# Optimization experiments

Hardware: AMD Instinct MI355X
Metric: run time of the kernel (lower is better)

## Reference

```python
import jax, jax.numpy as jnp
import numpy as np

B, T, D_IN, H, D_OUT = 64, 512, 256, 1024, 256


def _gru_cell(x, h, Wi, Wh, bi, bh):
    # x: [B, in_dim], h: [B, H]; Wi: [3H, in_dim], Wh: [3H, H]
    gi = x @ Wi.T + bi  # [B, 3H]
    gh = h @ Wh.T + bh  # [B, 3H]
    i_r, i_z, i_n = jnp.split(gi, 3, axis=-1)
    h_r, h_z, h_n = jnp.split(gh, 3, axis=-1)
    r = jax.nn.sigmoid(i_r + h_r)
    z = jax.nn.sigmoid(i_z + h_z)
    n = jnp.tanh(i_n + r * h_n)
    return (1.0 - z) * n + z * h


def setup_inputs() -> dict:
    key = jax.random.key(0)
    ks = jax.random.split(key, 11)
    s_in = 1.0 / np.sqrt(D_IN)
    s_h = 1.0 / np.sqrt(H)
    return {
        "x": jax.random.normal(ks[0], (B, T, D_IN), jnp.float32),
        "Wi0": jax.random.normal(ks[1], (3 * H, D_IN), jnp.float32) * s_in,
        "Wh0": jax.random.normal(ks[2], (3 * H, H), jnp.float32) * s_h,
        "bi0": jax.random.normal(ks[3], (3 * H,), jnp.float32) * s_h,
        "bh0": jax.random.normal(ks[4], (3 * H,), jnp.float32) * s_h,
        "Wi1": jax.random.normal(ks[5], (3 * H, H), jnp.float32) * s_h,
        "Wh1": jax.random.normal(ks[6], (3 * H, H), jnp.float32) * s_h,
        "bi1": jax.random.normal(ks[7], (3 * H,), jnp.float32) * s_h,
        "bh1": jax.random.normal(ks[8], (3 * H,), jnp.float32) * s_h,
        "Wo": jax.random.normal(ks[9], (D_OUT, H), jnp.float32) * s_h,
        "bo": jax.random.normal(ks[10], (D_OUT,), jnp.float32) * s_h,
    }


def reference(x, Wi0, Wh0, bi0, bh0, Wi1, Wh1, bi1, bh1, Wo, bo):
    b = x.shape[0]
    h0 = jnp.zeros((b, H), x.dtype)
    h1 = jnp.zeros((b, H), x.dtype)

    def step(carry, x_t):
        h0, h1 = carry
        h0 = _gru_cell(x_t, h0, Wi0, Wh0, bi0, bh0)
        h1 = _gru_cell(h0, h1, Wi1, Wh1, bi1, bh1)
        return (h0, h1), None

    (h0, h1), _ = jax.lax.scan(step, (h0, h1), jnp.swapaxes(x, 0, 1))
    return h1 @ Wo.T + bo  # [B, D_OUT]
```

## Files before the change

### kernel.cpp

```cpp
#include <hip/hip_runtime.h>

constexpr int kB    = 64;
constexpr int kT    = 512;
constexpr int kDin  = 256;
constexpr int kH    = 1024;
constexpr int kH3   = 3072;
constexpr int kDout = 256;
constexpr int kHB   = kB * kH;

typedef float  f32x4  __attribute__((ext_vector_type(4)));
typedef __bf16 bf16x8 __attribute__((ext_vector_type(8)));
typedef unsigned u32x4 __attribute__((ext_vector_type(4)));
typedef unsigned long long u64;

__device__ __forceinline__ float b2f(unsigned short u) {
  union { float f; unsigned u32; } c; c.u32 = ((unsigned)u) << 16; return c.f;
}
__device__ __forceinline__ unsigned short f2b(float f) {
  union { float f; unsigned u32; } c; c.f = f;
  unsigned r = c.u32 + 0x7fffu + ((c.u32 >> 16) & 1u);
  return (unsigned short)(r >> 16);
}
__device__ __forceinline__ bf16x8 ld8(const unsigned short* p) {
  return *reinterpret_cast<const bf16x8*>(p);
}
__device__ __forceinline__ u64 ald(const u64* p) {
  return __hip_atomic_load(p, __ATOMIC_RELAXED, __HIP_MEMORY_SCOPE_AGENT);
}
__device__ __forceinline__ unsigned ald32(const unsigned* p) {
  return __hip_atomic_load(p, __ATOMIC_RELAXED, __HIP_MEMORY_SCOPE_AGENT);
}
__device__ __forceinline__ void ast32(unsigned* p, unsigned v) {
  __hip_atomic_store(p, v, __ATOMIC_RELAXED, __HIP_MEMORY_SCOPE_AGENT);
}
__device__ __forceinline__ float sigm_(float x) { return 1.f / (1.f + __expf(-x)); }
__device__ __forceinline__ float tanh_(float x) {
  return 1.f - 2.f / (__expf(2.f * x) + 1.f);
}

#define MFMA16(a, b, c) __builtin_amdgcn_mfma_f32_16x16x32_bf16((a), (b), (c), 0, 0, 0)

__device__ __forceinline__ int swzcol(int C, int quad) {
  return (C & ~63) + ((quad ^ (((C >> 3) ^ (C >> 6)) & 7)) << 3);
}

__global__ void gru_prep(const float* __restrict__ x,
                         const float* __restrict__ Wi0, const float* __restrict__ Wh0,
                         const float* __restrict__ bi0, const float* __restrict__ bh0,
                         const float* __restrict__ Wi1, const float* __restrict__ Wh1,
                         const float* __restrict__ bi1, const float* __restrict__ bh1,
                         unsigned short* __restrict__ xb,
                         unsigned short* __restrict__ wi0b, unsigned short* __restrict__ wh0b,
                         unsigned short* __restrict__ wi1b, unsigned short* __restrict__ wh1b,
                         unsigned short* __restrict__ r0, unsigned short* __restrict__ r1,
                         float* __restrict__ bias, unsigned* __restrict__ sync) {
  const int stride = gridDim.x * blockDim.x;
  const int g = blockIdx.x * blockDim.x + threadIdx.x;
  for (int i = g; i < kH3 * kDin; i += stride) wi0b[i] = f2b(Wi0[i]);
  for (int i = g; i < kH3 * kH; i += stride) {
    wh0b[i] = f2b(Wh0[i]); wi1b[i] = f2b(Wi1[i]); wh1b[i] = f2b(Wh1[i]);
  }
  for (int i = g; i < kB * kT * kDin; i += stride) xb[i] = f2b(x[i]);
  for (int i = g; i < kHB; i += stride) { r0[i] = 0; r1[i] = 0; }
  for (int i = g; i < kH; i += stride) {
    bias[0 * kH + i] = bi0[0 * kH + i] + bh0[0 * kH + i];
    bias[1 * kH + i] = bi0[1 * kH + i] + bh0[1 * kH + i];
    bias[2 * kH + i] = bi0[2 * kH + i];
    bias[3 * kH + i] = bh0[2 * kH + i];
    bias[4 * kH + i] = bi1[0 * kH + i] + bh1[0 * kH + i];
    bias[5 * kH + i] = bi1[1 * kH + i] + bh1[1 * kH + i];
    bias[6 * kH + i] = bi1[2 * kH + i];
    bias[7 * kH + i] = bh1[2 * kH + i];
  }
  for (int i = g; i < 4096; i += stride) sync[i] = 0;
}

__global__ void __launch_bounds__(256, 1) gru_main(
    const unsigned short* __restrict__ xb,
    const unsigned short* __restrict__ wi0, const unsigned short* __restrict__ wh0,
    const unsigned short* __restrict__ wi1, const unsigned short* __restrict__ wh1,
    const float* __restrict__ bias,
    unsigned short* __restrict__ r0, unsigned short* __restrict__ r1,
    unsigned* __restrict__ sync, const int rmode,
    const float* __restrict__ Wo, const float* __restrict__ bo,
    float* __restrict__ out) {
  __shared__ unsigned short hl0[16][1032];
  __shared__ unsigned short hl1[16][1032];
  __shared__ float red[2][4][64][5];
  __shared__ bf16x8 wlds[2][32][64];

  const int tid  = threadIdx.x;
  const int lane = tid & 63;
  const int wv   = tid >> 6;
  const int ln15 = lane & 15;
  const int quad = lane >> 4;

  const int xcd   = blockIdx.x & 7;
  const int rest  = blockIdx.x >> 3;
  const int jsub  = rest & 7;
  const int mtile = rest >> 3;
  const int pidx  = xcd * 8 + jsub;

  const int layer = wv >> 1;
  const int kh    = wv & 1;
  const int jrow  = xcd * 128 + jsub * 16 + ln15;
  const int jcol  = jrow;

  const unsigned short *pw_r, *pw_z, *pw_n, *pv_r, *pv_z, *pv_n;
  if (layer == 0) {
    pw_r = wh0 + (size_t)(0 * kH + jrow) * kH + kh * 512 + quad * 8;
    pw_z = wh0 + (size_t)(1 * kH + jrow) * kH + kh * 512 + quad * 8;
    pw_n = wh0 + (size_t)(2 * kH + jrow) * kH + kh * 512 + quad * 8;
    pv_r = wi0 + (size_t)(0 * kH + jrow) * kDin + kh * 128 + quad * 8;
    pv_z = wi0 + (size_t)(1 * kH + jrow) * kDin + kh * 128 + quad * 8;
    pv_n = wi0 + (size_t)(2 * kH + jrow) * kDin + kh * 128 + quad * 8;
  } else {
    pw_r = wh1 + (size_t)(0 * kH + jrow) * kH + kh * 512 + quad * 8;
    pw_z = wh1 + (size_t)(1 * kH + jrow) * kH + kh * 512 + quad * 8;
    pw_n = wh1 + (size_t)(2 * kH + jrow) * kH + kh * 512 + quad * 8;
    pv_r = wi1 + (size_t)(0 * kH + jrow) * kH + kh * 512 + quad * 8;
    pv_z = wi1 + (size_t)(1 * kH + jrow) * kH + kh * 512 + quad * 8;
    pv_n = wi1 + (size_t)(2 * kH + jrow) * kH + kh * 512 + quad * 8;
  }

  const float* bb = bias + layer * 4 * kH;
  const float b_r = bb[jcol];
  const float b_z = bb[kH + jcol];
  const float b_i = bb[2 * kH + jcol];
  const float b_h = bb[3 * kH + jcol];

  bf16x8 W[64];
  if (layer == 0) {
#pragma unroll
    for (int kk = 0; kk < 16; ++kk) {
      W[kk]      = ld8(pw_r + kk * 32);
      W[16 + kk] = ld8(pw_z + kk * 32);
      W[32 + kk] = ld8(pw_n + kk * 32);
    }
#pragma unroll
    for (int kk = 0; kk < 4; ++kk) {
      W[48 + kk] = ld8(pv_r + kk * 32);
      W[52 + kk] = ld8(pv_z + kk * 32);
      W[56 + kk] = ld8(pv_n + kk * 32);
    }
  } else {
#pragma unroll
    for (int kk = 0; kk < 16; ++kk) {
      W[kk]      = ld8(pv_r + kk * 32);
      W[16 + kk] = ld8(pv_z + kk * 32);
      W[32 + kk] = ld8(pv_n + kk * 32);
      W[48 + kk] = ld8(pw_r + kk * 32);
      wlds[kh][kk][lane]      = ld8(pw_z + kk * 32);
      wlds[kh][16 + kk][lane] = ld8(pw_n + kk * 32);
    }
  }

  const f32x4 z4 = {0.f, 0.f, 0.f, 0.f};
  unsigned* fl0 = sync + (size_t)xcd * 512 + mtile * 64;
  unsigned* fl1 = sync + (size_t)xcd * 512 + 256 + mtile * 64;

  float hprev[4] = {0.f, 0.f, 0.f, 0.f};

  for (int t = 0; t <= kT; ++t) {
    const bool l0c = (t < kT);
    const bool l1c = (t >= 1);
    const int s0r = rmode ? t : (t & 1);
    const int s0w = rmode ? (t + 1) : ((t + 1) & 1);
    const int s1r = rmode ? (t >= 1 ? t - 1 : 0) : ((t >= 1 ? t - 1 : 0) & 1);
    const int s1w = rmode ? t : (t & 1);

    f32x4 a_r = z4, a_z = z4, a_i = z4, a_h = z4;

    if (layer == 0 && l0c) {
      const unsigned short* xp = xb + (size_t)(mtile * 16 + ln15) * (kT * kDin) +
                                 t * kDin + kh * 128 + quad * 8;
      bf16x8 xa[4];
#pragma unroll
      for (int i = 0; i < 4; ++i) xa[i] = ld8(xp + i * 32);
#pragma unroll
      for (int kk = 0; kk < 4; ++kk) {
        a_r = MFMA16(xa[kk], W[48 + kk], a_r);
        a_z = MFMA16(xa[kk], W[52 + kk], a_z);
        a_i = MFMA16(xa[kk], W[56 + kk], a_i);
      }
    }

    if (wv == 0) {
      int missed = 0;
      for (;;) {
        int a = (int)ald32(fl0 + lane);
        int b = (int)ald32(fl1 + lane);
        if (__all(a >= t && b >= t - 1)) break;
        if (!missed) { __builtin_amdgcn_s_sleep(16); missed = 1; }
        else         { __builtin_amdgcn_s_sleep(4); }
      }
    }
    __syncthreads();

    {
      const int r = tid >> 4, s = tid & 15;
      const unsigned short* b0 =
          r0 + (size_t)s0r * kHB + (size_t)(mtile * 16 + r) * kH + s * 64;
      const unsigned short* b1 =
          r1 + (size_t)s1r * kHB + (size_t)(mtile * 16 + r) * kH + s * 64;
      if (rmode) {
        u32x4 d0[8], d1[8];
#pragma unroll
        for (int i = 0; i < 8; ++i) d0[i] = *(const u32x4*)(b0 + i * 8);
#pragma unroll
        for (int i = 0; i < 8; ++i) d1[i] = *(const u32x4*)(b1 + i * 8);
#pragma unroll
        for (int i = 0; i < 8; ++i)
          *(u32x4*)&hl0[r][s * 64 + ((i ^ s) & 7) * 8] = d0[i];
#pragma unroll
        for (int i = 0; i < 8; ++i)
          *(u32x4*)&hl1[r][s * 64 + ((i ^ s) & 7) * 8] = d1[i];
      } else {
        u64 w0[16], w1[16];
#pragma unroll
        for (int i = 0; i < 16; ++i) w0[i] = ald((const u64*)b0 + i);
#pragma unroll
        for (int i = 0; i < 16; ++i) w1[i] = ald((const u64*)b1 + i);
#pragma unroll
        for (int i = 0; i < 16; ++i)
          *(u64*)&hl0[r][s * 64 + (((i >> 1) ^ s) & 7) * 8 + (i & 1) * 4] = w0[i];
#pragma unroll
        for (int i = 0; i < 16; ++i)
          *(u64*)&hl1[r][s * 64 + (((i >> 1) ^ s) & 7) * 8 + (i & 1) * 4] = w1[i];
      }
    }
    __syncthreads();

    const bool active = (layer == 0) ? l0c : l1c;
    if (active) {
      const int kb = kh * 512;
      if (layer == 0) {
#pragma unroll
        for (int kk = 0; kk < 16; ++kk) {
          bf16x8 A = *(const bf16x8*)&hl0[ln15][swzcol(kb + kk * 32, quad)];
          a_r = MFMA16(A, W[kk], a_r);
          a_z = MFMA16(A, W[16 + kk], a_z);
          a_h = MFMA16(A, W[32 + kk], a_h);
        }
      } else {
#pragma unroll
        for (int kk = 0; kk < 16; ++kk) {
          bf16x8 A0 = *(const bf16x8*)&hl0[ln15][swzcol(kb + kk * 32, quad)];
          a_r = MFMA16(A0, W[kk], a_r);
          a_z = MFMA16(A0, W[16 + kk], a_z);
          a_i = MFMA16(A0, W[32 + kk], a_i);
          bf16x8 A1 = *(const bf16x8*)&hl1[ln15][swzcol(kb + kk * 32, quad)];
          a_r = MFMA16(A1, W[48 + kk], a_r);
          a_z = MFMA16(A1, wlds[kh][kk][lane], a_z);
          a_h = MFMA16(A1, wlds[kh][16 + kk][lane], a_h);
        }
      }
    }

    if (((wv == 1) && l0c) || ((wv == 3) && l1c)) {
#pragma unroll
      for (int q = 0; q < 4; ++q) {
        red[layer][0][lane][q] = a_r[q]; red[layer][1][lane][q] = a_z[q];
        red[layer][2][lane][q] = a_i[q]; red[layer][3][lane][q] = a_h[q];
      }
    }
    __syncthreads();

    if (((wv == 0) && l0c) || ((wv == 2) && l1c)) {
      float hv4[4];
#pragma unroll
      for (int q = 0; q < 4; ++q) {
        float sr = a_r[q] + red[layer][0][lane][q];
        float sz = a_z[q] + red[layer][1][lane][q];
        float si = a_i[q] + red[layer][2][lane][q];
        float sh = a_h[q] + red[layer][3][lane][q];
        float rg = sigm_(sr + b_r);
        float zg = sigm_(sz + b_z);
        float ng = tanh_(si + b_i + rg * (sh + b_h));
        hv4[q] = (1.f - zg) * ng + zg * hprev[q];
        hprev[q] = hv4[q];
      }
      unsigned short* dst = (layer == 0) ? r0 + (size_t)s0w * kHB
                                         : r1 + (size_t)s1w * kHB;
#pragma unroll
      for (int q = 0; q < 4; ++q) {
        float pv = __shfl_xor(hv4[q], 1);
        if (!(lane & 1)) {
          unsigned pk = (unsigned)f2b(hv4[q]) | ((unsigned)f2b(pv) << 16);
          unsigned* d = (unsigned*)(dst + (size_t)(mtile * 16 + quad * 4 + q) * kH +
                                    (jcol & ~1));
          ast32(d, pk);
        }
      }
      asm volatile("s_waitcnt vmcnt(0)" ::: "memory");
      if (lane == 0) {
        const int base = (layer == 0) ? (mtile * 64 + pidx)
                                      : (256 + mtile * 64 + pidx);
        const unsigned val = (layer == 0) ? (unsigned)(t + 1) : (unsigned)t;
#pragma unroll
        for (int r8 = 0; r8 < 8; ++r8) ast32(sync + r8 * 512 + base, val);
      }
    }
  }

  if (wv == 0) {
    int missed = 0;
    for (;;) {
      int f = (int)ald32(fl1 + lane);
      if (__all(f >= (int)kT)) break;
      if (!missed) { __builtin_amdgcn_s_sleep(16); missed = 1; }
      else         { __builtin_amdgcn_s_sleep(4); }
    }
  }
  __syncthreads();
  {
    const int sfin = rmode ? kT : 0;
    const int r = tid >> 4, s = tid & 15;
    const unsigned short* b1 =
        r1 + (size_t)sfin * kHB + (size_t)(mtile * 16 + r) * kH + s * 64;
    if (rmode) {
      u32x4 d[8];
#pragma unroll
      for (int i = 0; i < 8; ++i) d[i] = *(const u32x4*)(b1 + i * 8);
#pragma unroll
      for (int i = 0; i < 8; ++i) *(u32x4*)&hl0[r][s * 64 + i * 8] = d[i];
    } else {
      u64 w[16];
#pragma unroll
      for (int i = 0; i < 16; ++i) w[i] = ald((const u64*)b1 + i);
#pragma unroll
      for (int i = 0; i < 16; ++i) *(u64*)&hl0[r][s * 64 + i * 4] = w[i];
    }
  }
  __syncthreads();
  {
    const int c  = tid & 31;
    const int rr = tid >> 5;
    const int col = jsub * 32 + c;
    const float* wr = Wo + (size_t)col * kH;
    float acc0 = bo[col], acc1 = bo[col];
#pragma unroll 8
    for (int k = 0; k < kH; k += 4) {
      float4 w4 = *reinterpret_cast<const float4*>(wr + k);
      acc0 += b2f(hl0[rr][k]) * w4.x + b2f(hl0[rr][k + 1]) * w4.y +
              b2f(hl0[rr][k + 2]) * w4.z + b2f(hl0[rr][k + 3]) * w4.w;
      acc1 += b2f(hl0[rr + 8][k]) * w4.x + b2f(hl0[rr + 8][k + 1]) * w4.y +
              b2f(hl0[rr + 8][k + 2]) * w4.z + b2f(hl0[rr + 8][k + 3]) * w4.w;
    }
    out[(mtile * 16 + rr) * kDout + col] = acc0;
    out[(mtile * 16 + rr + 8) * kDout + col] = acc1;
  }
}

extern "C" void kernel_launch(void* const* d_in, const int* in_sizes, int n_in,
                              void* d_out, int out_size, void* d_ws, size_t ws_size,
                              hipStream_t stream) {
  const float* x   = (const float*)d_in[0];
  const float* Wi0 = (const float*)d_in[1];
  const float* Wh0 = (const float*)d_in[2];
  const float* bi0 = (const float*)d_in[3];
  const float* bh0 = (const float*)d_in[4];
  const float* Wi1 = (const float*)d_in[5];
  const float* Wh1 = (const float*)d_in[6];
  const float* bi1 = (const float*)d_in[7];
  const float* bh1 = (const float*)d_in[8];
  const float* Wo  = (const float*)d_in[9];
  const float* bo  = (const float*)d_in[10];

  char* ws = (char*)d_ws;
  size_t off = 0;
  auto take = [&](size_t bytes) {
    size_t r = off;
    off += (bytes + 255) & ~(size_t)255;
    return r;
  };
  unsigned short* xb   = (unsigned short*)(ws + take((size_t)kB * kT * kDin * 2));
  unsigned short* wi0b = (unsigned short*)(ws + take((size_t)kH3 * kDin * 2));
  unsigned short* wh0b = (unsigned short*)(ws + take((size_t)kH3 * kH * 2));
  unsigned short* wi1b = (unsigned short*)(ws + take((size_t)kH3 * kH * 2));
  unsigned short* wh1b = (unsigned short*)(ws + take((size_t)kH3 * kH * 2));
  float*          bias = (float*)(ws + take(8 * kH * sizeof(float)));
  unsigned*       sync = (unsigned*)(ws + take(4096 * sizeof(unsigned)));

  const size_t slot_b = (size_t)kHB * 2;
  int rmode = 1;
  size_t ring_slots = (size_t)kT + 1;
  if (off + 2 * (ring_slots * slot_b) + (1u << 20) > ws_size) {
    rmode = 0;
    ring_slots = 2;
  }
  unsigned short* r0 = (unsigned short*)(ws + take(ring_slots * slot_b));
  unsigned short* r1 = (unsigned short*)(ws + take(ring_slots * slot_b));

  gru_prep<<<2048, 256, 0, stream>>>(x, Wi0, Wh0, bi0, bh0, Wi1, Wh1, bi1, bh1,
                                     xb, wi0b, wh0b, wi1b, wh1b, r0, r1, bias,
                                     sync);
  gru_main<<<256, 256, 0, stream>>>(xb, wi0b, wh0b, wi1b, wh1b, bias, r0, r1,
                                    sync, rmode, Wo, bo, (float*)d_out);
}
```

Before: 3.319 ms.

## Tile hidden-state buffers per producer block and poll flags in every wave

Changes the global layout of the recurrent hidden-state ring buffers so each producer block writes a contiguous 16x16 tile (mtile*16384 + pidx*256) instead of strided rows. The staging into LDS is rewritten to read these tiles with a matching swizzle. Every wave now spins on the sync flags itself, which removes the __syncthreads that followed the wave-0 poll, and the sleep intervals are shortened. Flag publication uses eight lanes in parallel instead of a serial loop in lane 0. The aim is to cut per-step synchronisation latency and get coalesced remote stores. The cost is more polling traffic from all waves and a swizzle that must stay consistent with the MFMA reads.

```diff
diff --git a/kernel.cpp b/kernel.cpp
--- a/kernel.cpp
+++ b/kernel.cpp
@@ -42,6 +42,42 @@
 
 __device__ __forceinline__ int swzcol(int C, int quad) {
   return (C & ~63) + ((quad ^ (((C >> 3) ^ (C >> 6)) & 7)) << 3);
+}
+
+__device__ __forceinline__ void stage_p(unsigned short (*hl)[1032],
+                                        const unsigned short* slotm,
+                                        int p, int rg, int rmode) {
+  const unsigned short* src = slotm + p * 256 + rg * 64;
+  const int cb = p * 2;
+  if (rmode) {
+    u32x4 d[8];
+#pragma unroll
+    for (int i = 0; i < 4; ++i) {
+      d[i * 2]     = *(const u32x4*)(src + i * 16);
+      d[i * 2 + 1] = *(const u32x4*)(src + i * 16 + 8);
+    }
+#pragma unroll
+    for (int i = 0; i < 4; ++i)
+#pragma unroll
+      for (int h = 0; h < 2; ++h) {
+        const int c  = cb + h;
+        const int so = ((c & ~7) | ((c ^ (c >> 3)) & 7)) * 8;
+        *(u32x4*)&hl[rg * 4 + i][so] = d[i * 2 + h];
+      }
+  } else {
+    u64 w[16];
+#pragma unroll
+    for (int i = 0; i < 16; ++i) w[i] = ald((const u64*)src + i);
+#pragma unroll
+    for (int i = 0; i < 4; ++i)
+#pragma unroll
+      for (int h = 0; h < 2; ++h) {
+        const int c  = cb + h;
+        const int so = ((c & ~7) | ((c ^ (c >> 3)) & 7)) * 8;
+        *(u64*)&hl[rg * 4 + i][so]     = w[i * 4 + h * 2];
+        *(u64*)&hl[rg * 4 + i][so + 4] = w[i * 4 + h * 2 + 1];
+      }
+  }
 }
 
 __global__ void gru_prep(const float* __restrict__ x,
@@ -161,6 +197,9 @@
 
   float hprev[4] = {0.f, 0.f, 0.f, 0.f};
 
+  const int sp  = tid & 63;
+  const int srg = tid >> 6;
+
   for (int t = 0; t <= kT; ++t) {
     const bool l0c = (t < kT);
     const bool l1c = (t >= 1);
@@ -185,50 +224,19 @@
       }
     }
 
-    if (wv == 0) {
-      int missed = 0;
+    {
+      int first = 1;
       for (;;) {
         int a = (int)ald32(fl0 + lane);
         int b = (int)ald32(fl1 + lane);
         if (__all(a >= t && b >= t - 1)) break;
-        if (!missed) { __builtin_amdgcn_s_sleep(16); missed = 1; }
-        else         { __builtin_amdgcn_s_sleep(4); }
-      }
-    }
-    __syncthreads();
-
-    {
-      const int r = tid >> 4, s = tid & 15;
-      const unsigned short* b0 =
-          r0 + (size_t)s0r * kHB + (size_t)(mtile * 16 + r) * kH + s * 64;
-      const unsigned short* b1 =
-          r1 + (size_t)s1r * kHB + (size_t)(mtile * 16 + r) * kH + s * 64;
-      if (rmode) {
-        u32x4 d0[8], d1[8];
-#pragma unroll
-        for (int i = 0; i < 8; ++i) d0[i] = *(const u32x4*)(b0 + i * 8);
-#pragma unroll
-        for (int i = 0; i < 8; ++i) d1[i] = *(const u32x4*)(b1 + i * 8);
-#pragma unroll
-        for (int i = 0; i < 8; ++i)
-          *(u32x4*)&hl0[r][s * 64 + ((i ^ s) & 7) * 8] = d0[i];
-#pragma unroll
-        for (int i = 0; i < 8; ++i)
-          *(u32x4*)&hl1[r][s * 64 + ((i ^ s) & 7) * 8] = d1[i];
-      } else {
-        u64 w0[16], w1[16];
-#pragma unroll
-        for (int i = 0; i < 16; ++i) w0[i] = ald((const u64*)b0 + i);
-#pragma unroll
-        for (int i = 0; i < 16; ++i) w1[i] = ald((const u64*)b1 + i);
-#pragma unroll
-        for (int i = 0; i < 16; ++i)
-          *(u64*)&hl0[r][s * 64 + (((i >> 1) ^ s) & 7) * 8 + (i & 1) * 4] = w0[i];
-#pragma unroll
-        for (int i = 0; i < 16; ++i)
-          *(u64*)&hl1[r][s * 64 + (((i >> 1) ^ s) & 7) * 8 + (i & 1) * 4] = w1[i];
-      }
-    }
+        if (first) { __builtin_amdgcn_s_sleep(8); first = 0; }
+        else       { __builtin_amdgcn_s_sleep(2); }
+      }
+    }
+
+    stage_p(hl0, r0 + (size_t)s0r * kHB + mtile * 16384, sp, srg, rmode);
+    stage_p(hl1, r1 + (size_t)s1r * kHB + mtile * 16384, sp, srg, rmode);
     __syncthreads();
 
     const bool active = (layer == 0) ? l0c : l1c;
@@ -280,56 +288,63 @@
         hv4[q] = (1.f - zg) * ng + zg * hprev[q];
         hprev[q] = hv4[q];
       }
-      unsigned short* dst = (layer == 0) ? r0 + (size_t)s0w * kHB
-                                         : r1 + (size_t)s1w * kHB;
+      unsigned short* dst = ((layer == 0) ? r0 + (size_t)s0w * kHB
+                                          : r1 + (size_t)s1w * kHB) +
+                            mtile * 16384 + pidx * 256;
 #pragma unroll
       for (int q = 0; q < 4; ++q) {
         float pv = __shfl_xor(hv4[q], 1);
         if (!(lane & 1)) {
           unsigned pk = (unsigned)f2b(hv4[q]) | ((unsigned)f2b(pv) << 16);
-          unsigned* d = (unsigned*)(dst + (size_t)(mtile * 16 + quad * 4 + q) * kH +
-                                    (jcol & ~1));
+          unsigned* d = (unsigned*)(dst + (quad * 4 + q) * 16 + (ln15 & ~1));
           ast32(d, pk);
         }
       }
       asm volatile("s_waitcnt vmcnt(0)" ::: "memory");
-      if (lane == 0) {
-        const int base = (layer == 0) ? (mtile * 64 + pidx)
-                                      : (256 + mtile * 64 + pidx);
-        const unsigned val = (layer == 0) ? (unsigned)(t + 1) : (unsigned)t;
-#pragma unroll
-        for (int r8 = 0; r8 < 8; ++r8) ast32(sync + r8 * 512 + base, val);
-      }
-    }
-  }
-
-  if (wv == 0) {
-    int missed = 0;
+      const int base = (layer == 0) ? (mtile * 64 + pidx)
+                                    : (256 + mtile * 64 + pidx);
+      const unsigned val = (layer == 0) ? (unsigned)(t + 1) : (unsigned)t;
+      if (lane < 8) ast32(sync + lane * 512 + base, val);
+    }
+  }
+
+  {
+    int first = 1;
     for (;;) {
       int f = (int)ald32(fl1 + lane);
       if (__all(f >= (int)kT)) break;
-      if (!missed) { __builtin_amdgcn_s_sleep(16); missed = 1; }
-      else         { __builtin_amdgcn_s_sleep(4); }
+      if (first) { __builtin_amdgcn_s_sleep(8); first = 0; }
+      else       { __builtin_amdgcn_s_sleep(2); }
     }
   }
   __syncthreads();
   {
     const int sfin = rmode ? kT : 0;
-    const int r = tid >> 4, s = tid & 15;
-    const unsigned short* b1 =
-        r1 + (size_t)sfin * kHB + (size_t)(mtile * 16 + r) * kH + s * 64;
+    const unsigned short* src =
+        r1 + (size_t)sfin * kHB + mtile * 16384 + sp * 256 + srg * 64;
     if (rmode) {
       u32x4 d[8];
 #pragma unroll
-      for (int i = 0; i < 8; ++i) d[i] = *(const u32x4*)(b1 + i * 8);
-#pragma unroll
-      for (int i = 0; i < 8; ++i) *(u32x4*)&hl0[r][s * 64 + i * 8] = d[i];
+      for (int i = 0; i < 4; ++i) {
+        d[i * 2]     = *(const u32x4*)(src + i * 16);
+        d[i * 2 + 1] = *(const u32x4*)(src + i * 16 + 8);
+      }
+#pragma unroll
+      for (int i = 0; i < 4; ++i) {
+        *(u32x4*)&hl0[srg * 4 + i][sp * 16]     = d[i * 2];
+        *(u32x4*)&hl0[srg * 4 + i][sp * 16 + 8] = d[i * 2 + 1];
+      }
     } else {
       u64 w[16];
 #pragma unroll
-      for (int i = 0; i < 16; ++i) w[i] = ald((const u64*)b1 + i);
-#pragma unroll
-      for (int i = 0; i < 16; ++i) *(u64*)&hl0[r][s * 64 + i * 4] = w[i];
+      for (int i = 0; i < 16; ++i) w[i] = ald((const u64*)src + i);
+#pragma unroll
+      for (int i = 0; i < 4; ++i) {
+        *(u64*)&hl0[srg * 4 + i][sp * 16]      = w[i * 4];
+        *(u64*)&hl0[srg * 4 + i][sp * 16 + 4]  = w[i * 4 + 1];
+        *(u64*)&hl0[srg * 4 + i][sp * 16 + 8]  = w[i * 4 + 2];
+        *(u64*)&hl0[srg * 4 + i][sp * 16 + 12] = w[i * 4 + 3];
+      }
     }
   }
   __syncthreads();
```

Measured after the change: 3.438 ms. 3.6% more time.

## Replace block-wide barriers with per-wave LDS flag handoffs in GRU time loop

Applied to the files above, without the earlier changes.

Removes the three __syncthreads per timestep and replaces them with fine-grained LDS producer/consumer flags between the four waves. Each wave now polls global sync flags itself and stages only its half of the hidden state. Layer-0 and layer-1 waves can therefore run decoupled within a step. In rmode, the global flag wait checks only the relevant 32 producer slots instead of all 64, and the sleep intervals are shortened. The risks are more complex ordering, duplicated polling traffic, and subtle races on the LDS buffers shared between layers.

```diff
diff --git a/kernel.cpp b/kernel.cpp
--- a/kernel.cpp
+++ b/kernel.cpp
@@ -42,6 +42,45 @@
 
 __device__ __forceinline__ int swzcol(int C, int quad) {
   return (C & ~63) + ((quad ^ (((C >> 3) ^ (C >> 6)) & 7)) << 3);
+}
+
+__device__ __forceinline__ void stage_seg(unsigned short* ldsrow,
+                                          const unsigned short* src, int s,
+                                          int rmode) {
+  if (rmode) {
+    u32x4 d[8];
+#pragma unroll
+    for (int i = 0; i < 8; ++i) d[i] = *(const u32x4*)(src + i * 8);
+#pragma unroll
+    for (int i = 0; i < 8; ++i)
+      *(u32x4*)&ldsrow[s * 64 + ((i ^ s) & 7) * 8] = d[i];
+  } else {
+    u64 w[16];
+#pragma unroll
+    for (int i = 0; i < 16; ++i) w[i] = ald((const u64*)src + i);
+#pragma unroll
+    for (int i = 0; i < 16; ++i)
+      *(u64*)&ldsrow[s * 64 + (((i >> 1) ^ s) & 7) * 8 + (i & 1) * 4] = w[i];
+  }
+}
+
+__device__ __forceinline__ void stage_half(unsigned short (*hl)[1032],
+                                           const unsigned short* rbase,
+                                           int kh, int lane, int rmode) {
+  const int r = lane >> 2;
+  const int s = kh * 8 + (lane & 3) * 2;
+  const unsigned short* src = rbase + (size_t)r * kH + s * 64;
+  stage_seg(hl[r], src, s, rmode);
+  stage_seg(hl[r], src + 64, s + 1, rmode);
+}
+
+__device__ __forceinline__ void pb_post(unsigned* p, unsigned v, int lane) {
+  if (lane == 0)
+    __hip_atomic_store(p, v, __ATOMIC_RELEASE, __HIP_MEMORY_SCOPE_WORKGROUP);
+}
+__device__ __forceinline__ void pb_wait(unsigned* p, unsigned v) {
+  while (__hip_atomic_load(p, __ATOMIC_ACQUIRE, __HIP_MEMORY_SCOPE_WORKGROUP) < v)
+    __builtin_amdgcn_s_sleep(1);
 }
 
 __global__ void gru_prep(const float* __restrict__ x,
@@ -88,6 +127,7 @@
   __shared__ unsigned short hl1[16][1032];
   __shared__ float red[2][4][64][5];
   __shared__ bf16x8 wlds[2][32][64];
+  __shared__ unsigned pb[8];
 
   const int tid  = threadIdx.x;
   const int lane = tid & 63;
@@ -155,6 +195,9 @@
     }
   }
 
+  if (tid < 8) pb[tid] = 0;
+  __syncthreads();
+
   const f32x4 z4 = {0.f, 0.f, 0.f, 0.f};
   unsigned* fl0 = sync + (size_t)xcd * 512 + mtile * 64;
   unsigned* fl1 = sync + (size_t)xcd * 512 + 256 + mtile * 64;
@@ -169,72 +212,46 @@
     const int s1r = rmode ? (t >= 1 ? t - 1 : 0) : ((t >= 1 ? t - 1 : 0) & 1);
     const int s1w = rmode ? t : (t & 1);
 
-    f32x4 a_r = z4, a_z = z4, a_i = z4, a_h = z4;
-
-    if (layer == 0 && l0c) {
-      const unsigned short* xp = xb + (size_t)(mtile * 16 + ln15) * (kT * kDin) +
-                                 t * kDin + kh * 128 + quad * 8;
-      bf16x8 xa[4];
-#pragma unroll
-      for (int i = 0; i < 4; ++i) xa[i] = ld8(xp + i * 32);
-#pragma unroll
-      for (int kk = 0; kk < 4; ++kk) {
-        a_r = MFMA16(xa[kk], W[48 + kk], a_r);
-        a_z = MFMA16(xa[kk], W[52 + kk], a_z);
-        a_i = MFMA16(xa[kk], W[56 + kk], a_i);
-      }
-    }
-
-    if (wv == 0) {
-      int missed = 0;
-      for (;;) {
-        int a = (int)ald32(fl0 + lane);
-        int b = (int)ald32(fl1 + lane);
-        if (__all(a >= t && b >= t - 1)) break;
-        if (!missed) { __builtin_amdgcn_s_sleep(16); missed = 1; }
-        else         { __builtin_amdgcn_s_sleep(4); }
-      }
-    }
-    __syncthreads();
-
-    {
-      const int r = tid >> 4, s = tid & 15;
-      const unsigned short* b0 =
-          r0 + (size_t)s0r * kHB + (size_t)(mtile * 16 + r) * kH + s * 64;
-      const unsigned short* b1 =
-          r1 + (size_t)s1r * kHB + (size_t)(mtile * 16 + r) * kH + s * 64;
-      if (rmode) {
-        u32x4 d0[8], d1[8];
-#pragma unroll
-        for (int i = 0; i < 8; ++i) d0[i] = *(const u32x4*)(b0 + i * 8);
-#pragma unroll
-        for (int i = 0; i < 8; ++i) d1[i] = *(const u32x4*)(b1 + i * 8);
-#pragma unroll
-        for (int i = 0; i < 8; ++i)
-          *(u32x4*)&hl0[r][s * 64 + ((i ^ s) & 7) * 8] = d0[i];
-#pragma unroll
-        for (int i = 0; i < 8; ++i)
-          *(u32x4*)&hl1[r][s * 64 + ((i ^ s) & 7) * 8] = d1[i];
-      } else {
-        u64 w0[16], w1[16];
-#pragma unroll
-        for (int i = 0; i < 16; ++i) w0[i] = ald((const u64*)b0 + i);
-#pragma unroll
-        for (int i = 0; i < 16; ++i) w1[i] = ald((const u64*)b1 + i);
-#pragma unroll
-        for (int i = 0; i < 16; ++i)
-          *(u64*)&hl0[r][s * 64 + (((i >> 1) ^ s) & 7) * 8 + (i & 1) * 4] = w0[i];
-#pragma unroll
-        for (int i = 0; i < 16; ++i)
-          *(u64*)&hl1[r][s * 64 + (((i >> 1) ^ s) & 7) * 8 + (i & 1) * 4] = w1[i];
-      }
-    }
-    __syncthreads();
-
-    const bool active = (layer == 0) ? l0c : l1c;
-    if (active) {
-      const int kb = kh * 512;
-      if (layer == 0) {
+    const unsigned short* r0base = r0 + (size_t)s0r * kHB + (size_t)(mtile * 16) * kH;
+    const unsigned short* r1base = r1 + (size_t)s1r * kHB + (size_t)(mtile * 16) * kH;
+    const int kb = kh * 512;
+
+    if (layer == 0) {
+      f32x4 a_r = z4, a_z = z4, a_i = z4, a_h = z4;
+      if (l0c) {
+        const unsigned short* xp = xb + (size_t)(mtile * 16 + ln15) * (kT * kDin) +
+                                   t * kDin + kh * 128 + quad * 8;
+        bf16x8 xa[4];
+#pragma unroll
+        for (int i = 0; i < 4; ++i) xa[i] = ld8(xp + i * 32);
+#pragma unroll
+        for (int kk = 0; kk < 4; ++kk) {
+          a_r = MFMA16(xa[kk], W[48 + kk], a_r);
+          a_z = MFMA16(xa[kk], W[52 + kk], a_z);
+          a_i = MFMA16(xa[kk], W[56 + kk], a_i);
+        }
+      }
+      {
+        int first = 1;
+        for (;;) {
+          bool ok;
+          if (rmode) {
+            int a = (int)ald32(fl0 + kh * 32 + (lane & 31));
+            ok = __all(a >= t);
+          } else {
+            int a = (int)ald32(fl0 + lane);
+            int b = (int)ald32(fl1 + lane);
+            ok = __all(a >= t && b >= t - 1);
+          }
+          if (ok) break;
+          if (first) { __builtin_amdgcn_s_sleep(8); first = 0; }
+          else       { __builtin_amdgcn_s_sleep(2); }
+        }
+      }
+      pb_wait(&pb[2 + kh], t);
+      stage_half(hl0, r0base, kh, lane, rmode);
+      pb_post(&pb[0 + kh], t + 1, lane);
+      if (l0c) {
 #pragma unroll
         for (int kk = 0; kk < 16; ++kk) {
           bf16x8 A = *(const bf16x8*)&hl0[ln15][swzcol(kb + kk * 32, quad)];
@@ -242,7 +259,72 @@
           a_z = MFMA16(A, W[16 + kk], a_z);
           a_h = MFMA16(A, W[32 + kk], a_h);
         }
+      }
+      if (kh == 0) {
+        pb_wait(&pb[4], t + 1);
+        if (l0c) {
+          float hv4[4];
+#pragma unroll
+          for (int q = 0; q < 4; ++q) {
+            float sr = a_r[q] + red[0][0][lane][q];
+            float sz = a_z[q] + red[0][1][lane][q];
+            float si = a_i[q] + red[0][2][lane][q];
+            float sh = a_h[q] + red[0][3][lane][q];
+            float rg = sigm_(sr + b_r);
+            float zg = sigm_(sz + b_z);
+            float ng = tanh_(si + b_i + rg * (sh + b_h));
+            hv4[q] = (1.f - zg) * ng + zg * hprev[q];
+            hprev[q] = hv4[q];
+          }
+          unsigned short* dst = r0 + (size_t)s0w * kHB;
+#pragma unroll
+          for (int q = 0; q < 4; ++q) {
+            float pv = __shfl_xor(hv4[q], 1);
+            if (!(lane & 1)) {
+              unsigned pk = (unsigned)f2b(hv4[q]) | ((unsigned)f2b(pv) << 16);
+              ast32((unsigned*)(dst + (size_t)(mtile * 16 + quad * 4 + q) * kH +
+                                (jcol & ~1)),
+                    pk);
+            }
+          }
+          asm volatile("s_waitcnt vmcnt(0)" ::: "memory");
+          if (lane < 8) ast32(sync + lane * 512 + mtile * 64 + pidx, (unsigned)(t + 1));
+        }
+        pb_post(&pb[6], t + 1, lane);
       } else {
+        pb_wait(&pb[6], t);
+        if (l0c) {
+#pragma unroll
+          for (int q = 0; q < 4; ++q) {
+            red[0][0][lane][q] = a_r[q]; red[0][1][lane][q] = a_z[q];
+            red[0][2][lane][q] = a_i[q]; red[0][3][lane][q] = a_h[q];
+          }
+        }
+        pb_post(&pb[4], t + 1, lane);
+      }
+    } else {
+      {
+        int first = 1;
+        for (;;) {
+          bool ok;
+          if (rmode) {
+            int a = (int)ald32(fl0 + kh * 32 + (lane & 31));
+            int b = (int)ald32(fl1 + kh * 32 + (lane & 31));
+            ok = __all(a >= t && b >= t - 1);
+          } else {
+            int a = (int)ald32(fl0 + lane);
+            int b = (int)ald32(fl1 + lane);
+            ok = __all(a >= t && b >= t - 1);
+          }
+          if (ok) break;
+          if (first) { __builtin_amdgcn_s_sleep(8); first = 0; }
+          else       { __builtin_amdgcn_s_sleep(2); }
+        }
+      }
+      stage_half(hl1, r1base, kh, lane, rmode);
+      pb_wait(&pb[0 + kh], t + 1);
+      f32x4 a_r = z4, a_z = z4, a_i = z4, a_h = z4;
+      if (l1c) {
 #pragma unroll
         for (int kk = 0; kk < 16; ++kk) {
           bf16x8 A0 = *(const bf16x8*)&hl0[ln15][swzcol(kb + kk * 32, quad)];
@@ -255,61 +337,60 @@
           a_h = MFMA16(A1, wlds[kh][16 + kk][lane], a_h);
         }
       }
-    }
-
-    if (((wv == 1) && l0c) || ((wv == 3) && l1c)) {
-#pragma unroll
-      for (int q = 0; q < 4; ++q) {
-        red[layer][0][lane][q] = a_r[q]; red[layer][1][lane][q] = a_z[q];
-        red[layer][2][lane][q] = a_i[q]; red[layer][3][lane][q] = a_h[q];
-      }
-    }
-    __syncthreads();
-
-    if (((wv == 0) && l0c) || ((wv == 2) && l1c)) {
-      float hv4[4];
-#pragma unroll
-      for (int q = 0; q < 4; ++q) {
-        float sr = a_r[q] + red[layer][0][lane][q];
-        float sz = a_z[q] + red[layer][1][lane][q];
-        float si = a_i[q] + red[layer][2][lane][q];
-        float sh = a_h[q] + red[layer][3][lane][q];
-        float rg = sigm_(sr + b_r);
-        float zg = sigm_(sz + b_z);
-        float ng = tanh_(si + b_i + rg * (sh + b_h));
-        hv4[q] = (1.f - zg) * ng + zg * hprev[q];
-        hprev[q] = hv4[q];
-      }
-      unsigned short* dst = (layer == 0) ? r0 + (size_t)s0w * kHB
-                                         : r1 + (size_t)s1w * kHB;
-#pragma unroll
-      for (int q = 0; q < 4; ++q) {
-        float pv = __shfl_xor(hv4[q], 1);
-        if (!(lane & 1)) {
-          unsigned pk = (unsigned)f2b(hv4[q]) | ((unsigned)f2b(pv) << 16);
-          unsigned* d = (unsigned*)(dst + (size_t)(mtile * 16 + quad * 4 + q) * kH +
-                                    (jcol & ~1));
-          ast32(d, pk);
-        }
-      }
-      asm volatile("s_waitcnt vmcnt(0)" ::: "memory");
-      if (lane == 0) {
-        const int base = (layer == 0) ? (mtile * 64 + pidx)
-                                      : (256 + mtile * 64 + pidx);
-        const unsigned val = (layer == 0) ? (unsigned)(t + 1) : (unsigned)t;
-#pragma unroll
-        for (int r8 = 0; r8 < 8; ++r8) ast32(sync + r8 * 512 + base, val);
+      pb_post(&pb[2 + kh], t + 1, lane);
+      if (kh == 0) {
+        pb_wait(&pb[5], t + 1);
+        if (l1c) {
+          float hv4[4];
+#pragma unroll
+          for (int q = 0; q < 4; ++q) {
+            float sr = a_r[q] + red[1][0][lane][q];
+            float sz = a_z[q] + red[1][1][lane][q];
+            float si = a_i[q] + red[1][2][lane][q];
+            float sh = a_h[q] + red[1][3][lane][q];
+            float rg = sigm_(sr + b_r);
+            float zg = sigm_(sz + b_z);
+            float ng = tanh_(si + b_i + rg * (sh + b_h));
+            hv4[q] = (1.f - zg) * ng + zg * hprev[q];
+            hprev[q] = hv4[q];
+          }
+          unsigned short* dst = r1 + (size_t)s1w * kHB;
+#pragma unroll
+          for (int q = 0; q < 4; ++q) {
+            float pv = __shfl_xor(hv4[q], 1);
+            if (!(lane & 1)) {
+              unsigned pk = (unsigned)f2b(hv4[q]) | ((unsigned)f2b(pv) << 16);
+              ast32((unsigned*)(dst + (size_t)(mtile * 16 + quad * 4 + q) * kH +
+                                (jcol & ~1)),
+                    pk);
+            }
+          }
+          asm volatile("s_waitcnt vmcnt(0)" ::: "memory");
+          if (lane < 8)
+            ast32(sync + lane * 512 + 256 + mtile * 64 + pidx, (unsigned)t);
+        }
+        pb_post(&pb[7], t + 1, lane);
+      } else {
+        pb_wait(&pb[7], t);
+        if (l1c) {
+#pragma unroll
+          for (int q = 0; q < 4; ++q) {
+            red[1][0][lane][q] = a_r[q]; red[1][1][lane][q] = a_z[q];
+            red[1][2][lane][q] = a_i[q]; red[1][3][lane][q] = a_h[q];
+          }
+        }
+        pb_post(&pb[5], t + 1, lane);
       }
     }
   }
 
   if (wv == 0) {
-    int missed = 0;
+    int first = 1;
     for (;;) {
       int f = (int)ald32(fl1 + lane);
       if (__all(f >= (int)kT)) break;
-      if (!missed) { __builtin_amdgcn_s_sleep(16); missed = 1; }
-      else         { __builtin_amdgcn_s_sleep(4); }
+      if (first) { __builtin_amdgcn_s_sleep(8); first = 0; }
+      else       { __builtin_amdgcn_s_sleep(2); }
     }
   }
   __syncthreads();
```

Measured after the change: 3.288 ms. No clear change (-0.9%).
